# Optimization experiments

Hardware: AMD Instinct MI355X
Metric: run time of the kernel (lower is better)

## Reference

```python
import jax, jax.numpy as jnp
import numpy as np

N_NODES = 20000
NUM_DRUGS = 2048
NUM_DPI = 200000
IN_C = 256
EMB = 256
HID = 512
OUT = 1
N_CL = 8
B = 16384


def setup_inputs() -> dict:
    key = jax.random.key(0)
    ks = jax.random.split(key, 10)
    x = jax.random.normal(ks[0], (N_NODES, IN_C), jnp.float32)
    # bipartite DPI edges: drug ids in [0, NUM_DRUGS), protein ids in [NUM_DRUGS, N_NODES)
    d = jax.random.randint(ks[1], (NUM_DPI,), 0, NUM_DRUGS)
    p = jax.random.randint(ks[2], (NUM_DPI,), NUM_DRUGS, N_NODES)
    edge_index = jnp.concatenate([jnp.stack([d, p]), jnp.stack([p, d])], axis=1)  # [2, 2*NUM_DPI]
    drug_drug_batch = jax.random.randint(ks[3], (2, B), 0, NUM_DRUGS)
    edge_cell_lines = jax.random.randint(ks[4], (B,), 0, N_CL)
    Wg1 = jax.random.normal(ks[5], (IN_C, EMB), jnp.float32) / np.float32(np.sqrt(IN_C))
    bg1 = jnp.zeros((EMB,), jnp.float32)
    Wg2 = jax.random.normal(ks[6], (EMB, EMB), jnp.float32) / np.float32(np.sqrt(EMB))
    bg2 = jnp.zeros((EMB,), jnp.float32)
    W1 = jax.random.normal(ks[7], (N_CL, 2 * EMB, HID), jnp.float32) / np.float32(np.sqrt(2 * EMB))
    b1 = jnp.zeros((N_CL, HID), jnp.float32)
    W2 = jax.random.normal(ks[8], (N_CL, HID, OUT), jnp.float32) / np.float32(np.sqrt(HID))
    b2 = jnp.zeros((N_CL, OUT), jnp.float32)
    return dict(x=x, edge_index=edge_index, drug_drug_batch=drug_drug_batch,
                edge_cell_lines=edge_cell_lines, num_drugs=NUM_DRUGS,
                Wg1=Wg1, bg1=bg1, Wg2=Wg2, bg2=bg2, W1=W1, b1=b1, W2=W2, b2=b2)


def _gcn(h_in, row, col, W, b, n):
    # PyG GCNConv: self-loops already appended to (row, col); symmetric normalization.
    h = h_in @ W  # [N, EMB]
    deg = jax.ops.segment_sum(jnp.ones(col.shape[0], h.dtype), col, num_segments=n)
    dinv = jnp.where(deg > 0, jax.lax.rsqrt(jnp.maximum(deg, 1e-12)), 0.0)
    msg = h[row] * (dinv[row] * dinv[col])[:, None]
    return jax.ops.segment_sum(msg, col, num_segments=n) + b


def reference(x, edge_index, drug_drug_batch, edge_cell_lines, num_drugs,
              Wg1, bg1, Wg2, bg2, W1, b1, W2, b2):
    n = x.shape[0]
    ar = jnp.arange(n, dtype=edge_index.dtype)
    row = jnp.concatenate([edge_index[0], ar])
    col = jnp.concatenate([edge_index[1], ar])
    h = jax.nn.relu(_gcn(x, row, col, Wg1, bg1, n))
    h = jax.nn.relu(_gcn(h, row, col, Wg2, bg2, n))
    # scatter-mean pool node embeddings of proteins into per-drug graph embeddings
    num_dpi = edge_index.shape[1] // 2
    avg = jnp.sort(edge_index[:, :num_dpi], axis=0)  # row0=drug id, row1=protein id
    node_emb = h[avg[1]]  # [NUM_DPI, EMB]
    sums = jax.ops.segment_sum(node_emb, avg[0], num_segments=num_drugs)
    cnt = jax.ops.segment_sum(jnp.ones(num_dpi, h.dtype), avg[0], num_segments=num_drugs)
    graph = sums / jnp.maximum(cnt, 1.0)[:, None]  # [NUM_DRUGS, EMB]
    xcat = jnp.concatenate([graph[drug_drug_batch[0]], graph[drug_drug_batch[1]]], axis=1)  # [B, 2*EMB]
    # per-cell-line MLP routing: run each expert over all rows, then gather per-row expert output
    n_cl = W1.shape[0]
    outs = jnp.stack([jax.nn.relu(xcat @ W1[c] + b1[c]) @ W2[c] + b2[c] for c in range(n_cl)])  # [C, B, OUT]
    preds = outs[edge_cell_lines, jnp.arange(xcat.shape[0])]  # [B, OUT]
    return preds
```

## Files before the change

kernel.cpp:

```cpp
#include <hip/hip_runtime.h>
#include <hip/hip_bf16.h>

#define N_NODES 20000
#define NUM_DRUGS 2048
#define N_PROT (N_NODES - NUM_DRUGS)
#define NUM_DPI 200000
#define E2 400000
#define CDIM 256
#define HID 512
#define N_CL 8
#define BATCH 16384
#define HN 8192

#define STRD 32
#define STRP 16
#define ELLD 192
#define ELLP 48

#define NB_T64 512
#define NB_TWG 32
#define NB_ZERO 79
#define NB_SPLIT 20000

#define MT_NODE 313

#define NB_AGG_D NUM_DRUGS
#define NB_AGG_P ((N_PROT + 3) / 4)

typedef __attribute__((ext_vector_type(8))) short short8;
typedef __attribute__((ext_vector_type(4))) float floatx4;

__device__ inline unsigned short f2bf(float f) {
    unsigned u = __float_as_uint(f);
    u += 0x7fff + ((u >> 16) & 1);
    return (unsigned short)(u >> 16);
}
__device__ inline float bf2f(unsigned short h) {
    return __uint_as_float((unsigned)h << 16);
}
__device__ inline void split2(float v, unsigned short& h, unsigned short& l) {
    h = f2bf(v);
    l = f2bf(v - bf2f(h));
}
__device__ inline void gload16(const void* g, void* l) {
    __builtin_amdgcn_global_load_lds(
        (const __attribute__((address_space(1))) void*)g,
        (__attribute__((address_space(3))) void*)l, 16, 0, 0);
}
__device__ inline float4 f4fma(float4 v, float s, float4 a) {
    a.x = fmaf(v.x, s, a.x); a.y = fmaf(v.y, s, a.y);
    a.z = fmaf(v.z, s, a.z); a.w = fmaf(v.w, s, a.w);
    return a;
}
__device__ inline float4 bf4(const unsigned short* p) {
    ushort4 q = *(const ushort4*)p;
    return make_float4(bf2f(q.x), bf2f(q.y), bf2f(q.z), bf2f(q.w));
}

__global__ __launch_bounds__(256) void prep_all(
        const float* __restrict__ x, unsigned short* __restrict__ xhi,
        unsigned short* __restrict__ xlo,
        const float* __restrict__ Wg1, const float* __restrict__ Wg2,
        unsigned short* __restrict__ wg1Th, unsigned short* __restrict__ wg1Tl,
        unsigned short* __restrict__ wg2Th, unsigned short* __restrict__ wg2Tl,
        const float* __restrict__ W1, unsigned short* __restrict__ W1Th,
        unsigned short* __restrict__ W1Tl,
        int* __restrict__ cur_d, int* __restrict__ cur_p) {
    __shared__ float ld[64 * 65];
    int b = blockIdx.x;
    int t = threadIdx.x;
    int tx = t & 63, ty = t >> 6;
    if (b < NB_T64) {
        int m = b >> 5;
        int k0 = (b & 3) * 64, n0 = ((b >> 2) & 7) * 64;
        const float* Wm = W1 + (size_t)m * CDIM * HID;
#pragma unroll
        for (int rr = 0; rr < 16; rr++) {
            int kl = rr * 4 + ty;
            ld[tx * 65 + kl] = Wm[(size_t)(k0 + kl) * HID + n0 + tx];
        }
        __syncthreads();
        size_t obase = (size_t)m * HID * CDIM;
#pragma unroll
        for (int rr = 0; rr < 16; rr++) {
            int nl = rr * 4 + ty;
            float v = ld[nl * 65 + tx];
            unsigned short h, l;
            split2(v, h, l);
            size_t o = obase + (size_t)(n0 + nl) * CDIM + k0 + tx;
            W1Th[o] = h;
            W1Tl[o] = l;
        }
        return;
    }
    b -= NB_T64;
    if (b < NB_TWG) {
        const float* W = (b >> 4) ? Wg2 : Wg1;
        unsigned short* hi = (b >> 4) ? wg2Th : wg1Th;
        unsigned short* lo = (b >> 4) ? wg2Tl : wg1Tl;
        int k0 = (b & 3) * 64, n0 = ((b >> 2) & 3) * 64;
#pragma unroll
        for (int rr = 0; rr < 16; rr++) {
            int kl = rr * 4 + ty;
            ld[tx * 65 + kl] = W[(size_t)(k0 + kl) * CDIM + n0 + tx];
        }
        __syncthreads();
#pragma unroll
        for (int rr = 0; rr < 16; rr++) {
            int nl = rr * 4 + ty;
            float v = ld[nl * 65 + tx];
            unsigned short h, l;
            split2(v, h, l);
            size_t o = (size_t)(n0 + nl) * CDIM + k0 + tx;
            hi[o] = h;
            lo[o] = l;
        }
        return;
    }
    b -= NB_TWG;
    if (b < NB_ZERO) {
        int i = b * 256 + t;
        if (i < N_NODES) cur_p[i * STRP] = 0;
        if (i < NUM_DRUGS) cur_d[i * STRD] = 0;
        return;
    }
    b -= NB_ZERO;
    {
        int i = b * 256 + t;
        unsigned short h, l;
        split2(x[i], h, l);
        xhi[i] = h;
        xlo[i] = l;
    }
}

__global__ void fill_ell(const int* __restrict__ ei, int* cur_d, int* adj_drug,
                         int* cur_p, int* adj_prot) {
    int e = blockIdx.x * blockDim.x + threadIdx.x;
    if (e >= NUM_DPI) return;
    int d = ei[e];
    int p = ei[E2 + e];
    int posd = atomicAdd(&cur_d[d * STRD], 1);
    int posp = atomicAdd(&cur_p[p * STRP], 1);
    if (posd < ELLD) adj_drug[d * ELLD + posd] = p;
    if (posp < ELLP) adj_prot[(size_t)p * ELLP + posp] = d;
}

template <int BM, int BN, int SWZ>
__global__ __launch_bounds__(256) void gemm_mfma(
        const unsigned short* __restrict__ Ahi, const unsigned short* __restrict__ Alo,
        const unsigned short* __restrict__ BThi, const unsigned short* __restrict__ BTlo,
        float* __restrict__ C, unsigned short* __restrict__ Cbf,
        int M, int K, int N, int mTiles,
        const int* __restrict__ cur_d, const int* __restrict__ cur_p,
        float* __restrict__ dinv) {
    if ((int)blockIdx.x >= mTiles) {
        int i = (((int)blockIdx.x - mTiles) * (int)gridDim.y + (int)blockIdx.y) * 256
                + (int)threadIdx.x;
        if (i < N_NODES) {
            int deg = (i < NUM_DRUGS) ? cur_d[i * STRD] : cur_p[i * STRP];
            dinv[i] = rsqrtf((float)(deg + 1));
        }
        return;
    }
    constexpr int MI = BM / 32;
    constexpr int NJ = BN / 32;
    __shared__ unsigned short sAh[2][BM * 32], sAl[2][BM * 32];
    __shared__ unsigned short sBh[2][BN * 32], sBl[2][BN * 32];
    int t = threadIdx.x;
    int wv = t >> 6, lane = t & 63, quad = lane >> 4, l15 = lane & 15;
    int bx = blockIdx.x, by = blockIdx.y;
    if constexpr (SWZ) {
        int w = by * 16 + bx;
        int xcd = w & 7, j = w >> 3;
        bx = j & 15;
        by = xcd * 8 + (j >> 4);
    }
    int m0 = bx * BM, n0 = by * BN;
    int m0w = (wv >> 1) * (BM / 2), n0w = (wv & 1) * (BN / 2);
    floatx4 zero = {0.f, 0.f, 0.f, 0.f};
    floatx4 acc[MI][NJ];
#pragma unroll
    for (int i = 0; i < MI; i++)
#pragma unroll
        for (int j = 0; j < NJ; j++) acc[i][j] = zero;

    auto STAGE = [&](int buf, int kk) {
#pragma unroll
        for (int s = t; s < BM * 4; s += 256) {
            int row = s >> 2, pos = s & 3;
            int ch = pos ^ ((row >> 1) & 3);
            int arow = m0 + row; if (arow > M - 1) arow = M - 1;
            size_t aoff = (size_t)arow * K + kk + ch * 8;
            gload16(Ahi + aoff, &sAh[buf][s * 8]);
            gload16(Alo + aoff, &sAl[buf][s * 8]);
        }
#pragma unroll
        for (int s = t; s < BN * 4; s += 256) {
            int row = s >> 2, pos = s & 3;
            int ch = pos ^ ((row >> 1) & 3);
            int brow = n0 + row; if (brow > N - 1) brow = N - 1;
            size_t boff = (size_t)brow * K + kk + ch * 8;
            gload16(BThi + boff, &sBh[buf][s * 8]);
            gload16(BTlo + boff, &sBl[buf][s * 8]);
        }
    };

    int nk = K >> 5;
    STAGE(0, 0);
    asm volatile("s_waitcnt vmcnt(0)" ::: "memory");
    __builtin_amdgcn_s_barrier();
    int cur = 0;
    for (int it = 0; it < nk; ++it) {
        if (it + 1 < nk) STAGE(cur ^ 1, (it + 1) << 5);
        short8 ah[MI], al[MI], bh[NJ], bl[NJ];
        int posq = quad ^ ((l15 >> 1) & 3);
#pragma unroll
        for (int i = 0; i < MI; i++) {
            int sl = (m0w + i * 16 + l15) * 4 + posq;
            ah[i] = *(const short8*)&sAh[cur][sl * 8];
            al[i] = *(const short8*)&sAl[cur][sl * 8];
        }
#pragma unroll
        for (int j = 0; j < NJ; j++) {
            int sl = (n0w + j * 16 + l15) * 4 + posq;
            bh[j] = *(const short8*)&sBh[cur][sl * 8];
            bl[j] = *(const short8*)&sBl[cur][sl * 8];
        }
#pragma unroll
        for (int i = 0; i < MI; i++)
#pragma unroll
            for (int j = 0; j < NJ; j++) {
                acc[i][j] = __builtin_amdgcn_mfma_f32_16x16x32_bf16(ah[i], bh[j], acc[i][j], 0, 0, 0);
                acc[i][j] = __builtin_amdgcn_mfma_f32_16x16x32_bf16(ah[i], bl[j], acc[i][j], 0, 0, 0);
                acc[i][j] = __builtin_amdgcn_mfma_f32_16x16x32_bf16(al[i], bh[j], acc[i][j], 0, 0, 0);
            }
        if (it + 1 < nk) {
            asm volatile("s_waitcnt vmcnt(0)" ::: "memory");
            __builtin_amdgcn_s_barrier();
            cur ^= 1;
        }
    }
#pragma unroll
    for (int i = 0; i < MI; i++) {
        int gr = m0 + m0w + i * 16 + quad * 4;
#pragma unroll
        for (int r = 0; r < 4; r++) {
            if (gr + r < M) {
#pragma unroll
                for (int j = 0; j < NJ; j++) {
                    size_t o = (size_t)(gr + r) * N + n0 + n0w + j * 16 + l15;
                    float v = acc[i][j][r];
                    if (C) C[o] = v;
                    if (Cbf) Cbf[o] = f2bf(v);
                }
            }
        }
    }
}

__global__ __launch_bounds__(256) void aggregate1(const unsigned short* __restrict__ tmpbf,
                                                  const int* __restrict__ cur_d,
                                                  const int* __restrict__ adj_drug,
                                                  const int* __restrict__ cur_p,
                                                  const int* __restrict__ adj_prot,
                                                  const float* __restrict__ dinv,
                                                  const float* __restrict__ bias,
                                                  unsigned short* __restrict__ outhi,
                                                  unsigned short* __restrict__ outlo) {
    __shared__ float4 red[4][64];
    int b = blockIdx.x;
    int lane = threadIdx.x & 63;
    if (b < NB_AGG_D) {
        int d = b;
        int w = threadIdx.x >> 6;
        const int* adj = adj_drug + (size_t)d * ELLD;
        int ecnt = cur_d[d * STRD];
        int e = ecnt < ELLD ? ecnt : ELLD;
        float4 a0 = make_float4(0.f, 0.f, 0.f, 0.f);
        float4 a1 = a0, a2 = a0, a3 = a0;
        int idx = w;
        for (; idx + 12 < e; idx += 16) {
            int j0 = adj[idx], j1 = adj[idx + 4], j2 = adj[idx + 8], j3 = adj[idx + 12];
            float d0 = dinv[j0], d1 = dinv[j1], d2 = dinv[j2], d3 = dinv[j3];
            float4 v0 = bf4(&tmpbf[(size_t)j0 * CDIM + lane * 4]);
            float4 v1 = bf4(&tmpbf[(size_t)j1 * CDIM + lane * 4]);
            float4 v2 = bf4(&tmpbf[(size_t)j2 * CDIM + lane * 4]);
            float4 v3 = bf4(&tmpbf[(size_t)j3 * CDIM + lane * 4]);
            a0 = f4fma(v0, d0, a0);
            a1 = f4fma(v1, d1, a1);
            a2 = f4fma(v2, d2, a2);
            a3 = f4fma(v3, d3, a3);
        }
        for (; idx < e; idx += 4) {
            int j = adj[idx];
            a0 = f4fma(bf4(&tmpbf[(size_t)j * CDIM + lane * 4]), dinv[j], a0);
        }
        a0.x = (a0.x + a1.x) + (a2.x + a3.x);
        a0.y = (a0.y + a1.y) + (a2.y + a3.y);
        a0.z = (a0.z + a1.z) + (a2.z + a3.z);
        a0.w = (a0.w + a1.w) + (a2.w + a3.w);
        red[w][lane] = a0;
        __syncthreads();
        if (w == 0) {
            float di = dinv[d];
            float4 r0 = red[0][lane], r1 = red[1][lane], r2 = red[2][lane], r3 = red[3][lane];
            float4 self = bf4(&tmpbf[(size_t)d * CDIM + lane * 4]);
            float4 acc;
            acc.x = (r0.x + r1.x) + (r2.x + r3.x) + self.x * di;
            acc.y = (r0.y + r1.y) + (r2.y + r3.y) + self.y * di;
            acc.z = (r0.z + r1.z) + (r2.z + r3.z) + self.z * di;
            acc.w = (r0.w + r1.w) + (r2.w + r3.w) + self.w * di;
            float4 bv = ((const float4*)bias)[lane];
            float4 r;
            r.x = fmaxf(fmaf(acc.x, di, bv.x), 0.f);
            r.y = fmaxf(fmaf(acc.y, di, bv.y), 0.f);
            r.z = fmaxf(fmaf(acc.z, di, bv.z), 0.f);
            r.w = fmaxf(fmaf(acc.w, di, bv.w), 0.f);
            ushort4 h, l;
            split2(r.x, h.x, l.x); split2(r.y, h.y, l.y);
            split2(r.z, h.z, l.z); split2(r.w, h.w, l.w);
            *(ushort4*)&outhi[(size_t)d * CDIM + lane * 4] = h;
            *(ushort4*)&outlo[(size_t)d * CDIM + lane * 4] = l;
        }
        return;
    }
    int i = NUM_DRUGS + (b - NB_AGG_D) * 4 + (threadIdx.x >> 6);
    if (i >= N_NODES) return;
    float di = dinv[i];
    float4 a0 = make_float4(0.f, 0.f, 0.f, 0.f);
    float4 a1 = a0, a2 = a0, a3 = a0;
    const int* adj = adj_prot + (size_t)i * ELLP;
    int e = cur_p[i * STRP];
    int idx = 0;
    for (; idx + 4 <= e; idx += 4) {
        int j0 = adj[idx + 0], j1 = adj[idx + 1];
        int j2 = adj[idx + 2], j3 = adj[idx + 3];
        float d0 = dinv[j0], d1 = dinv[j1], d2 = dinv[j2], d3 = dinv[j3];
        float4 v0 = bf4(&tmpbf[(size_t)j0 * CDIM + lane * 4]);
        float4 v1 = bf4(&tmpbf[(size_t)j1 * CDIM + lane * 4]);
        float4 v2 = bf4(&tmpbf[(size_t)j2 * CDIM + lane * 4]);
        float4 v3 = bf4(&tmpbf[(size_t)j3 * CDIM + lane * 4]);
        a0 = f4fma(v0, d0, a0);
        a1 = f4fma(v1, d1, a1);
        a2 = f4fma(v2, d2, a2);
        a3 = f4fma(v3, d3, a3);
    }
    for (; idx < e; idx++) {
        int j = adj[idx];
        a0 = f4fma(bf4(&tmpbf[(size_t)j * CDIM + lane * 4]), dinv[j], a0);
    }
    float4 self = bf4(&tmpbf[(size_t)i * CDIM + lane * 4]);
    float4 acc;
    acc.x = (a0.x + a1.x) + (a2.x + a3.x) + self.x * di;
    acc.y = (a0.y + a1.y) + (a2.y + a3.y) + self.y * di;
    acc.z = (a0.z + a1.z) + (a2.z + a3.z) + self.z * di;
    acc.w = (a0.w + a1.w) + (a2.w + a3.w) + self.w * di;
    float4 bv = ((const float4*)bias)[lane];
    float4 r;
    r.x = fmaxf(fmaf(acc.x, di, bv.x), 0.f);
    r.y = fmaxf(fmaf(acc.y, di, bv.y), 0.f);
    r.z = fmaxf(fmaf(acc.z, di, bv.z), 0.f);
    r.w = fmaxf(fmaf(acc.w, di, bv.w), 0.f);
    ushort4 h, l;
    split2(r.x, h.x, l.x); split2(r.y, h.y, l.y);
    split2(r.z, h.z, l.z); split2(r.w, h.w, l.w);
    *(ushort4*)&outhi[(size_t)i * CDIM + lane * 4] = h;
    *(ushort4*)&outlo[(size_t)i * CDIM + lane * 4] = l;
}

__global__ __launch_bounds__(256) void aggregate2p(const unsigned short* __restrict__ t2bf,
                                                   const int* __restrict__ cur_p,
                                                   const int* __restrict__ adj_prot,
                                                   const float* __restrict__ dinv,
                                                   const float* __restrict__ bias,
                                                   unsigned short* __restrict__ h2bf) {
    int w = (blockIdx.x * blockDim.x + threadIdx.x) >> 6;
    int lane = threadIdx.x & 63;
    if (w >= N_PROT) return;
    int i = NUM_DRUGS + w;
    float di = dinv[i];
    float4 a0 = make_float4(0.f, 0.f, 0.f, 0.f);
    float4 a1 = a0, a2 = a0, a3 = a0;
    const int* adj = adj_prot + (size_t)i * ELLP;
    int e = cur_p[i * STRP];
    int idx = 0;
    for (; idx + 4 <= e; idx += 4) {
        int j0 = adj[idx + 0], j1 = adj[idx + 1];
        int j2 = adj[idx + 2], j3 = adj[idx + 3];
        float d0 = dinv[j0], d1 = dinv[j1], d2 = dinv[j2], d3 = dinv[j3];
        float4 v0 = bf4(&t2bf[(size_t)j0 * CDIM + lane * 4]);
        float4 v1 = bf4(&t2bf[(size_t)j1 * CDIM + lane * 4]);
        float4 v2 = bf4(&t2bf[(size_t)j2 * CDIM + lane * 4]);
        float4 v3 = bf4(&t2bf[(size_t)j3 * CDIM + lane * 4]);
        a0 = f4fma(v0, d0, a0);
        a1 = f4fma(v1, d1, a1);
        a2 = f4fma(v2, d2, a2);
        a3 = f4fma(v3, d3, a3);
    }
    for (; idx < e; idx++) {
        int j = adj[idx];
        a0 = f4fma(bf4(&t2bf[(size_t)j * CDIM + lane * 4]), dinv[j], a0);
    }
    float4 self = bf4(&t2bf[(size_t)i * CDIM + lane * 4]);
    float4 acc;
    acc.x = (a0.x + a1.x) + (a2.x + a3.x) + self.x * di;
    acc.y = (a0.y + a1.y) + (a2.y + a3.y) + self.y * di;
    acc.z = (a0.z + a1.z) + (a2.z + a3.z) + self.z * di;
    acc.w = (a0.w + a1.w) + (a2.w + a3.w) + self.w * di;
    float4 bv = ((const float4*)bias)[lane];
    ushort4 o;
    o.x = f2bf(fmaxf(fmaf(acc.x, di, bv.x), 0.f));
    o.y = f2bf(fmaxf(fmaf(acc.y, di, bv.y), 0.f));
    o.z = f2bf(fmaxf(fmaf(acc.z, di, bv.z), 0.f));
    o.w = f2bf(fmaxf(fmaf(acc.w, di, bv.w), 0.f));
    *(ushort4*)&h2bf[(size_t)i * CDIM + lane * 4] = o;
}

__global__ __launch_bounds__(256) void pool_drugs(const unsigned short* __restrict__ h2bf,
                                                  unsigned short* __restrict__ Ghi,
                                                  unsigned short* __restrict__ Glo,
                                                  const int* __restrict__ cur_d,
                                                  const int* __restrict__ adj_drug) {
    __shared__ float4 red[4][64];
    int d = blockIdx.x;
    int w = threadIdx.x >> 6, lane = threadIdx.x & 63;
    const int* adj = adj_drug + (size_t)d * ELLD;
    int ecnt = cur_d[d * STRD];
    int e = ecnt < ELLD ? ecnt : ELLD;
    float4 a0 = make_float4(0.f, 0.f, 0.f, 0.f);
    float4 a1 = a0, a2 = a0, a3 = a0;
    int idx = w;
    for (; idx + 12 < e; idx += 16) {
        int j0 = adj[idx], j1 = adj[idx + 4], j2 = adj[idx + 8], j3 = adj[idx + 12];
        float4 v0 = bf4(&h2bf[(size_t)j0 * CDIM + lane * 4]);
        float4 v1 = bf4(&h2bf[(size_t)j1 * CDIM + lane * 4]);
        float4 v2 = bf4(&h2bf[(size_t)j2 * CDIM + lane * 4]);
        float4 v3 = bf4(&h2bf[(size_t)j3 * CDIM + lane * 4]);
        a0.x += v0.x; a0.y += v0.y; a0.z += v0.z; a0.w += v0.w;
        a1.x += v1.x; a1.y += v1.y; a1.z += v1.z; a1.w += v1.w;
        a2.x += v2.x; a2.y += v2.y; a2.z += v2.z; a2.w += v2.w;
        a3.x += v3.x; a3.y += v3.y; a3.z += v3.z; a3.w += v3.w;
    }
    for (; idx < e; idx += 4) {
        float4 v = bf4(&h2bf[(size_t)adj[idx] * CDIM + lane * 4]);
        a0.x += v.x; a0.y += v.y; a0.z += v.z; a0.w += v.w;
    }
    a0.x = (a0.x + a1.x) + (a2.x + a3.x);
    a0.y = (a0.y + a1.y) + (a2.y + a3.y);
    a0.z = (a0.z + a1.z) + (a2.z + a3.z);
    a0.w = (a0.w + a1.w) + (a2.w + a3.w);
    red[w][lane] = a0;
    __syncthreads();
    if (w == 0) {
        float4 r0 = red[0][lane], r1 = red[1][lane], r2 = red[2][lane], r3 = red[3][lane];
        float4 acc;
        acc.x = (r0.x + r1.x) + (r2.x + r3.x);
        acc.y = (r0.y + r1.y) + (r2.y + r3.y);
        acc.z = (r0.z + r1.z) + (r2.z + r3.z);
        acc.w = (r0.w + r1.w) + (r2.w + r3.w);
        float sc = 1.f / (float)(ecnt > 1 ? ecnt : 1);
        acc.x *= sc; acc.y *= sc; acc.z *= sc; acc.w *= sc;
        ushort4 h, l;
        split2(acc.x, h.x, l.x); split2(acc.y, h.y, l.y);
        split2(acc.z, h.z, l.z); split2(acc.w, h.w, l.w);
        *(ushort4*)&Ghi[(size_t)d * CDIM + lane * 4] = h;
        *(ushort4*)&Glo[(size_t)d * CDIM + lane * 4] = l;
    }
}

__global__ __launch_bounds__(256) void mlp_out(const unsigned short* __restrict__ Hbf,
                                               const int* __restrict__ ddb,
                                               const int* __restrict__ ecl,
                                               const float* __restrict__ b1,
                                               const float* __restrict__ W2,
                                               const float* __restrict__ b2,
                                               float* __restrict__ outp) {
    int r = (blockIdx.x * blockDim.x + threadIdx.x) >> 6;
    int lane = threadIdx.x & 63;
    if (r >= BATCH) return;
    int c = ecl[r];
    int d0 = ddb[r], d1 = ddb[BATCH + r];
    int n = lane * 8;
    const unsigned short* h0 = Hbf + (size_t)d0 * HN + (size_t)(c * 2) * HID + n;
    const unsigned short* h1 = Hbf + (size_t)d1 * HN + (size_t)(c * 2 + 1) * HID + n;
    const float* b1e = b1 + (size_t)c * HID + n;
    const float* w2e = W2 + (size_t)c * HID + n;
    short8 a8 = *(const short8*)h0;
    short8 b8 = *(const short8*)h1;
    float4 bb0 = *(const float4*)(b1e);
    float4 bb1 = *(const float4*)(b1e + 4);
    float4 w0 = *(const float4*)(w2e);
    float4 w1 = *(const float4*)(w2e + 4);
    float s = 0.f;
    float h;
    h = bf2f((unsigned short)a8[0]) + bf2f((unsigned short)b8[0]) + bb0.x;
    s = fmaf(fmaxf(h, 0.f), w0.x, s);
    h = bf2f((unsigned short)a8[1]) + bf2f((unsigned short)b8[1]) + bb0.y;
    s = fmaf(fmaxf(h, 0.f), w0.y, s);
    h = bf2f((unsigned short)a8[2]) + bf2f((unsigned short)b8[2]) + bb0.z;
    s = fmaf(fmaxf(h, 0.f), w0.z, s);
    h = bf2f((unsigned short)a8[3]) + bf2f((unsigned short)b8[3]) + bb0.w;
    s = fmaf(fmaxf(h, 0.f), w0.w, s);
    h = bf2f((unsigned short)a8[4]) + bf2f((unsigned short)b8[4]) + bb1.x;
    s = fmaf(fmaxf(h, 0.f), w1.x, s);
    h = bf2f((unsigned short)a8[5]) + bf2f((unsigned short)b8[5]) + bb1.y;
    s = fmaf(fmaxf(h, 0.f), w1.y, s);
    h = bf2f((unsigned short)a8[6]) + bf2f((unsigned short)b8[6]) + bb1.z;
    s = fmaf(fmaxf(h, 0.f), w1.z, s);
    h = bf2f((unsigned short)a8[7]) + bf2f((unsigned short)b8[7]) + bb1.w;
    s = fmaf(fmaxf(h, 0.f), w1.w, s);
    s += __shfl_xor(s, 1);
    s += __shfl_xor(s, 2);
    s += __shfl_xor(s, 4);
    s += __shfl_xor(s, 8);
    s += __shfl_xor(s, 16);
    s += __shfl_xor(s, 32);
    if (lane == 0) outp[r] = s + b2[c];
}

extern "C" void kernel_launch(void* const* d_in, const int* in_sizes, int n_in,
                              void* d_out, int out_size, void* d_ws, size_t ws_size,
                              hipStream_t stream) {
    const float* x   = (const float*)d_in[0];
    const int* ei    = (const int*)d_in[1];
    const int* ddb   = (const int*)d_in[2];
    const int* ecl   = (const int*)d_in[3];
    const float* Wg1 = (const float*)d_in[5];
    const float* bg1 = (const float*)d_in[6];
    const float* Wg2 = (const float*)d_in[7];
    const float* bg2 = (const float*)d_in[8];
    const float* W1  = (const float*)d_in[9];
    const float* b1  = (const float*)d_in[10];
    const float* W2  = (const float*)d_in[11];
    const float* b2  = (const float*)d_in[12];
    float* outp = (float*)d_out;

    const size_t NC = (size_t)N_NODES * CDIM;
    const size_t HRES = (size_t)NUM_DRUGS * HN * sizeof(float);
    char* r0 = (char*)d_ws;
    unsigned short* Hbf   = (unsigned short*)d_ws;
    unsigned short* t2bf  = (unsigned short*)r0;
    unsigned short* t1bf  = (unsigned short*)(r0 + 20480000);
    unsigned short* h2bf  = t1bf;
    unsigned short* h1hi  = (unsigned short*)(r0 + 30720000);
    unsigned short* h1lo  = (unsigned short*)(r0 + 40960000);
    unsigned short* xhi   = h1hi;
    unsigned short* xlo   = h1lo;
    char* p = r0 + 51200000;
    auto alloc = [&](size_t bytes) {
        char* r = p;
        p += (bytes + 255) & ~size_t(255);
        return (void*)r;
    };
    float* dinv    = (float*)alloc(sizeof(float) * N_NODES);
    int* cur_d     = (int*)alloc(sizeof(int) * NUM_DRUGS * STRD);
    int* cur_p     = (int*)alloc(sizeof(int) * N_NODES * STRP);
    int* adj_drug  = (int*)alloc(sizeof(int) * NUM_DRUGS * ELLD);
    int* adj_prot  = (int*)alloc(sizeof(int) * (size_t)N_NODES * ELLP);
    p = (char*)d_ws + ((HRES + 255) & ~size_t(255));
    unsigned short* Ghi   = (unsigned short*)alloc(2 * NUM_DRUGS * CDIM);
    unsigned short* Glo   = (unsigned short*)alloc(2 * NUM_DRUGS * CDIM);
    unsigned short* wg1Th = (unsigned short*)alloc(2 * CDIM * CDIM);
    unsigned short* wg1Tl = (unsigned short*)alloc(2 * CDIM * CDIM);
    unsigned short* wg2Th = (unsigned short*)alloc(2 * CDIM * CDIM);
    unsigned short* wg2Tl = (unsigned short*)alloc(2 * CDIM * CDIM);
    unsigned short* W1Th  = (unsigned short*)alloc(2 * (size_t)N_CL * HID * HID);
    unsigned short* W1Tl  = (unsigned short*)alloc(2 * (size_t)N_CL * HID * HID);

    prep_all<<<NB_T64 + NB_TWG + NB_ZERO + NB_SPLIT, 256, 0, stream>>>(
        x, xhi, xlo, Wg1, Wg2, wg1Th, wg1Tl, wg2Th, wg2Tl, W1, W1Th, W1Tl,
        cur_d, cur_p);
    fill_ell<<<(NUM_DPI + 255) / 256, 256, 0, stream>>>(ei, cur_d, adj_drug,
                                                        cur_p, adj_prot);
    gemm_mfma<64, 128, 0><<<dim3(MT_NODE + 40, 2), 256, 0, stream>>>(
        xhi, xlo, wg1Th, wg1Tl, nullptr, t1bf, N_NODES, CDIM, CDIM,
        MT_NODE, cur_d, cur_p, dinv);
    aggregate1<<<NB_AGG_D + NB_AGG_P, 256, 0, stream>>>(
        t1bf, cur_d, adj_drug, cur_p, adj_prot, dinv, bg1, h1hi, h1lo);
    gemm_mfma<64, 128, 0><<<dim3(MT_NODE, 2), 256, 0, stream>>>(
        h1hi, h1lo, wg2Th, wg2Tl, nullptr, t2bf, N_NODES, CDIM, CDIM,
        MT_NODE, nullptr, nullptr, nullptr);
    aggregate2p<<<(N_PROT * 64 + 255) / 256, 256, 0, stream>>>(
        t2bf, cur_p, adj_prot, dinv, bg2, h2bf);
    pool_drugs<<<NUM_DRUGS, 256, 0, stream>>>(h2bf, Ghi, Glo, cur_d, adj_drug);
    gemm_mfma<128, 128, 1><<<dim3(NUM_DRUGS / 128, HN / 128), 256, 0, stream>>>(
        Ghi, Glo, W1Th, W1Tl, nullptr, Hbf, NUM_DRUGS, CDIM, HN,
        NUM_DRUGS / 128, nullptr, nullptr, nullptr);
    mlp_out<<<(BATCH * 64) / 256, 256, 0, stream>>>(Hbf, ddb, ecl, b1, W2, b2, outp);
}
```

Baseline: 249.5 us.

## Fuse ELL fill into prep kernel and add XCD-aware swizzle for node GEMMs

Moves the edge-list ELL fill into the prep_all launch and splits the count zeroing into its own small kernel. The fill runs concurrently with weight transposes and x splitting instead of in a separate launch, so the number of launches on the stream stays the same but more independent work shares one grid. Node GEMMs now use a 1D grid with a swizzle that keeps both N-halves of each M-tile, and contiguous M-tiles, on the same XCD for better L2 reuse. Padded blocks that map past the last tile exit early. The dinv computation in the first GEMM uses the trailing 79 blocks of the 1D grid.

```diff
diff --git a/kernel.cpp b/kernel.cpp
--- a/kernel.cpp
+++ b/kernel.cpp
@@ -17,12 +17,13 @@
 #define ELLD 192
 #define ELLP 48
 
+#define NB_FILL 782
 #define NB_T64 512
 #define NB_TWG 32
-#define NB_ZERO 79
 #define NB_SPLIT 20000
 
 #define MT_NODE 313
+#define NB_GNODE 640
 
 #define NB_AGG_D NUM_DRUGS
 #define NB_AGG_P ((N_PROT + 3) / 4)
@@ -57,19 +58,40 @@
     return make_float4(bf2f(q.x), bf2f(q.y), bf2f(q.z), bf2f(q.w));
 }
 
+__global__ void zero_counts(int* cur_d, int* cur_p) {
+    int i = blockIdx.x * blockDim.x + threadIdx.x;
+    if (i < N_NODES) cur_p[i * STRP] = 0;
+    if (i < NUM_DRUGS) cur_d[i * STRD] = 0;
+}
+
 __global__ __launch_bounds__(256) void prep_all(
+        const int* __restrict__ ei, int* __restrict__ cur_d,
+        int* __restrict__ adj_drug, int* __restrict__ cur_p,
+        int* __restrict__ adj_prot,
         const float* __restrict__ x, unsigned short* __restrict__ xhi,
         unsigned short* __restrict__ xlo,
         const float* __restrict__ Wg1, const float* __restrict__ Wg2,
         unsigned short* __restrict__ wg1Th, unsigned short* __restrict__ wg1Tl,
         unsigned short* __restrict__ wg2Th, unsigned short* __restrict__ wg2Tl,
         const float* __restrict__ W1, unsigned short* __restrict__ W1Th,
-        unsigned short* __restrict__ W1Tl,
-        int* __restrict__ cur_d, int* __restrict__ cur_p) {
+        unsigned short* __restrict__ W1Tl) {
     __shared__ float ld[64 * 65];
     int b = blockIdx.x;
     int t = threadIdx.x;
     int tx = t & 63, ty = t >> 6;
+    if (b < NB_FILL) {
+        int e = b * 256 + t;
+        if (e < NUM_DPI) {
+            int d = ei[e];
+            int p = ei[E2 + e];
+            int posd = atomicAdd(&cur_d[d * STRD], 1);
+            int posp = atomicAdd(&cur_p[p * STRP], 1);
+            if (posd < ELLD) adj_drug[d * ELLD + posd] = p;
+            if (posp < ELLP) adj_prot[(size_t)p * ELLP + posp] = d;
+        }
+        return;
+    }
+    b -= NB_FILL;
     if (b < NB_T64) {
         int m = b >> 5;
         int k0 = (b & 3) * 64, n0 = ((b >> 2) & 7) * 64;
@@ -118,13 +140,6 @@
         return;
     }
     b -= NB_TWG;
-    if (b < NB_ZERO) {
-        int i = b * 256 + t;
-        if (i < N_NODES) cur_p[i * STRP] = 0;
-        if (i < NUM_DRUGS) cur_d[i * STRD] = 0;
-        return;
-    }
-    b -= NB_ZERO;
     {
         int i = b * 256 + t;
         unsigned short h, l;
@@ -132,18 +147,6 @@
         xhi[i] = h;
         xlo[i] = l;
     }
-}
-
-__global__ void fill_ell(const int* __restrict__ ei, int* cur_d, int* adj_drug,
-                         int* cur_p, int* adj_prot) {
-    int e = blockIdx.x * blockDim.x + threadIdx.x;
-    if (e >= NUM_DPI) return;
-    int d = ei[e];
-    int p = ei[E2 + e];
-    int posd = atomicAdd(&cur_d[d * STRD], 1);
-    int posp = atomicAdd(&cur_p[p * STRP], 1);
-    if (posd < ELLD) adj_drug[d * ELLD + posd] = p;
-    if (posp < ELLP) adj_prot[(size_t)p * ELLP + posp] = d;
 }
 
 template <int BM, int BN, int SWZ>
@@ -170,11 +173,18 @@
     int t = threadIdx.x;
     int wv = t >> 6, lane = t & 63, quad = lane >> 4, l15 = lane & 15;
     int bx = blockIdx.x, by = blockIdx.y;
-    if constexpr (SWZ) {
+    if constexpr (SWZ == 1) {
         int w = by * 16 + bx;
         int xcd = w & 7, j = w >> 3;
         bx = j & 15;
         by = xcd * 8 + (j >> 4);
+    }
+    if constexpr (SWZ == 2) {
+        int id = bx;
+        int xcd = id & 7, k = id >> 3;
+        by = k & 1;
+        bx = xcd * 40 + (k >> 1);
+        if (bx >= MT_NODE) return;
     }
     int m0 = bx * BM, n0 = by * BN;
     int m0w = (wv >> 1) * (BM / 2), n0w = (wv & 1) * (BN / 2);
@@ -568,19 +578,18 @@
     unsigned short* W1Th  = (unsigned short*)alloc(2 * (size_t)N_CL * HID * HID);
     unsigned short* W1Tl  = (unsigned short*)alloc(2 * (size_t)N_CL * HID * HID);
 
-    prep_all<<<NB_T64 + NB_TWG + NB_ZERO + NB_SPLIT, 256, 0, stream>>>(
-        x, xhi, xlo, Wg1, Wg2, wg1Th, wg1Tl, wg2Th, wg2Tl, W1, W1Th, W1Tl,
-        cur_d, cur_p);
-    fill_ell<<<(NUM_DPI + 255) / 256, 256, 0, stream>>>(ei, cur_d, adj_drug,
-                                                        cur_p, adj_prot);
-    gemm_mfma<64, 128, 0><<<dim3(MT_NODE + 40, 2), 256, 0, stream>>>(
+    zero_counts<<<(N_NODES + 255) / 256, 256, 0, stream>>>(cur_d, cur_p);
+    prep_all<<<NB_FILL + NB_T64 + NB_TWG + NB_SPLIT, 256, 0, stream>>>(
+        ei, cur_d, adj_drug, cur_p, adj_prot,
+        x, xhi, xlo, Wg1, Wg2, wg1Th, wg1Tl, wg2Th, wg2Tl, W1, W1Th, W1Tl);
+    gemm_mfma<64, 128, 2><<<dim3(NB_GNODE + 79, 1), 256, 0, stream>>>(
         xhi, xlo, wg1Th, wg1Tl, nullptr, t1bf, N_NODES, CDIM, CDIM,
-        MT_NODE, cur_d, cur_p, dinv);
+        NB_GNODE, cur_d, cur_p, dinv);
     aggregate1<<<NB_AGG_D + NB_AGG_P, 256, 0, stream>>>(
         t1bf, cur_d, adj_drug, cur_p, adj_prot, dinv, bg1, h1hi, h1lo);
-    gemm_mfma<64, 128, 0><<<dim3(MT_NODE, 2), 256, 0, stream>>>(
+    gemm_mfma<64, 128, 2><<<dim3(NB_GNODE, 1), 256, 0, stream>>>(
         h1hi, h1lo, wg2Th, wg2Tl, nullptr, t2bf, N_NODES, CDIM, CDIM,
-        MT_NODE, nullptr, nullptr, nullptr);
+        NB_GNODE, nullptr, nullptr, nullptr);
     aggregate2p<<<(N_PROT * 64 + 255) / 256, 256, 0, stream>>>(
         t2bf, cur_p, adj_prot, dinv, bg2, h2bf);
     pool_drugs<<<NUM_DRUGS, 256, 0, stream>>>(h2bf, Ghi, Glo, cur_d, adj_drug);
```

After: 249.8 us. Within noise of the previous version (+0.1%).
